# Kernel optimization log

Measured on AMD Instinct MI355X. Metric: run time of the kernel, lower is better.

Reference implementation:

```python
import jax, jax.numpy as jnp
import numpy as np

B, IMG, P, CIN, D, L, H, HID = 64, 224, 16, 3, 768, 12, 12, 3072
HD = D // H                      # 64 head dim
N = (IMG // P) ** 2 + 1          # 197 tokens (cls + patches)
EQ = 1.0 / np.sqrt(D)            # EqualLinear scale (lr_mul=1)


def _ln(x):
    # LayerNorm(eps=1e-3, elementwise_affine=False)
    m = jnp.mean(x, axis=-1, keepdims=True)
    v = jnp.var(x, axis=-1, keepdims=True)
    return (x - m) * jax.lax.rsqrt(v + 1e-3)


def _smln(x, latent, gw, gb, bw, bb):
    # SelfModulatedLayerNorm: param-free LN then per-sample affine from latent
    gamma = (latent @ (gw * EQ).T + gb)[:, None, :]
    beta = (latent @ (bw * EQ).T + bb)[:, None, :]
    return _ln(x) * (1.0 + gamma) + beta


def _attention(x, qkvw, projw, projb):
    b, n, d = x.shape
    qkv = (x @ qkvw.T).reshape(b, n, 3, H, HD).transpose(2, 0, 3, 1, 4)  # [3,B,H,N,hd]
    q, k, v = qkv[0], qkv[1], qkv[2]
    attn = jax.nn.softmax(jnp.einsum('bhqd,bhkd->bhqk', q, k) * (HD ** -0.5), axis=-1)
    out = jnp.einsum('bhqk,bhkd->bhqd', attn, v).transpose(0, 2, 1, 3).reshape(b, n, d)
    return out @ projw.T + projb


def _forward(x, latent, conv_w, conv_b, cls_token, pos_embed,
             g1w, g1b, b1w, b1b, qkvw, projw, projb,
             g2w, g2b, b2w, b2b, fc1w, fc1b, fc2w, fc2b,
             gnw, gnb, bnw, bnb):
    b = x.shape[0]
    # PatchEmbed: conv stride=patch, flatten, transpose, sin activation
    feat = jax.lax.conv_general_dilated(
        x, conv_w, (P, P), 'VALID',
        dimension_numbers=('NCHW', 'OIHW', 'NCHW')) + conv_b[None, :, None, None]
    tok = jnp.sin(feat.reshape(b, D, -1).transpose(0, 2, 1))          # [B,196,D]
    tok = jnp.concatenate([jnp.broadcast_to(cls_token, (b, 1, D)), tok], axis=1)
    tok = tok + pos_embed                                             # [B,197,D]

    def block(t, p):
        (g1w_, g1b_, b1w_, b1b_, qkvw_, projw_, projb_,
         g2w_, g2b_, b2w_, b2b_, fc1w_, fc1b_, fc2w_, fc2b_) = p
        xn = _smln(t, latent, g1w_, g1b_, b1w_, b1b_)
        y = _attention(xn, qkvw_, projw_, projb_) + xn
        t = xn + y                       # source Block: x reassigned to norm1 output
        t = _smln(t, latent, g2w_, g2b_, b2w_, b2b_)
        h = jax.nn.gelu(t @ fc1w_.T + fc1b_, approximate=False)
        t = (h @ fc2w_.T + fc2b_) + t
        return t, None

    tok, _ = jax.lax.scan(block, tok, (g1w, g1b, b1w, b1b, qkvw, projw, projb,
                                       g2w, g2b, b2w, b2b, fc1w, fc1b, fc2w, fc2b))
    return _smln(tok, latent, gnw, gnb, bnw, bnb)


def setup_inputs() -> dict:
    key = jax.random.key(0)
    ks = jax.random.split(key, 20)
    r = lambda k, shape: 0.02 * jax.random.normal(k, shape, dtype=jnp.float32)
    z = lambda shape: jnp.zeros(shape, jnp.float32)
    return {
        'x': jax.random.normal(ks[0], (B, CIN, IMG, IMG), dtype=jnp.float32),
        'latent': jax.random.normal(ks[1], (B, D), dtype=jnp.float32),
        'conv_w': r(ks[2], (D, CIN, P, P)), 'conv_b': z((D,)),
        'cls_token': z((1, 1, D)), 'pos_embed': r(ks[3], (1, N, D)),
        'g1w': r(ks[4], (L, D, D)), 'g1b': z((L, D)),
        'b1w': r(ks[5], (L, D, D)), 'b1b': z((L, D)),
        'qkvw': r(ks[6], (L, 3 * D, D)),
        'projw': r(ks[7], (L, D, D)), 'projb': z((L, D)),
        'g2w': r(ks[8], (L, D, D)), 'g2b': z((L, D)),
        'b2w': r(ks[9], (L, D, D)), 'b2b': z((L, D)),
        'fc1w': r(ks[10], (L, HID, D)), 'fc1b': z((L, HID)),
        'fc2w': r(ks[11], (L, D, HID)), 'fc2b': z((L, D)),
        'gnw': r(ks[12], (D, D)), 'gnb': z((D,)),
        'bnw': r(ks[13], (D, D)), 'bnb': z((D,)),
    }


def reference(x, latent, conv_w, conv_b, cls_token, pos_embed,
              g1w, g1b, b1w, b1b, qkvw, projw, projb,
              g2w, g2b, b2w, b2b, fc1w, fc1b, fc2w, fc2b,
              gnw, gnb, bnw, bnb):
    return _forward(x, latent, conv_w, conv_b, cls_token, pos_embed,
                    g1w, g1b, b1w, b1b, qkvw, projw, projb,
                    g2w, g2b, b2w, b2b, fc1w, fc1b, fc2w, fc2b,
                    gnw, gnb, bnw, bnb)
```

## Files before the change

### kernel.cpp

```cpp
#include <hip/hip_runtime.h>

typedef unsigned short u16;
typedef __bf16 bf16x8 __attribute__((ext_vector_type(8)));
typedef unsigned short u16x8 __attribute__((ext_vector_type(8)));
typedef float f32x4 __attribute__((ext_vector_type(4)));

#define B_    64
#define NTOK  197
#define DIM   768
#define NH    12
#define LAY   12
#define HID_  3072
#define MROWS (B_*NTOK)

#define EPI_BF16  0
#define EPI_PROJ  2
#define EPI_GELU  3
#define EPI_FC2   4
#define EPI_PATCH 5

__device__ __forceinline__ u16 f2bf(float f) {
  unsigned u = __float_as_uint(f);
  u += 0x7FFFu + ((u >> 16) & 1u);
  return (u16)(u >> 16);
}
__device__ __forceinline__ float bf2f(u16 h) {
  return __uint_as_float(((unsigned)h) << 16);
}

__device__ __forceinline__ void gld_lds16(const void* g, void* l) {
  __builtin_amdgcn_global_load_lds(
      (const __attribute__((address_space(1))) void*)g,
      (__attribute__((address_space(3))) void*)l, 16, 0, 0);
}

__global__ void fill_k(float* __restrict__ o, float v, int n) {
  int i = blockIdx.x * blockDim.x + threadIdx.x;
  const int st = gridDim.x * blockDim.x;
  for (; i < n; i += st) o[i] = v;
}

__global__ void cvt_bf16(const float* __restrict__ in, u16* __restrict__ out, int n4) {
  int i = blockIdx.x * blockDim.x + threadIdx.x;
  const int st = gridDim.x * blockDim.x;
  for (; i < n4; i += st) {
    float4 v = ((const float4*)in)[i];
    ushort4 o;
    o.x = f2bf(v.x); o.y = f2bf(v.y); o.z = f2bf(v.z); o.w = f2bf(v.w);
    ((ushort4*)out)[i] = o;
  }
}

__global__ void cvt4_k(const float* __restrict__ s0, const float* __restrict__ s1,
                       const float* __restrict__ s2, const float* __restrict__ s3,
                       u16* __restrict__ d0, u16* __restrict__ d1,
                       u16* __restrict__ d2, u16* __restrict__ d3,
                       int n0, int n1, int n2, int n3)
{
  int i = blockIdx.x * blockDim.x + threadIdx.x;
  const int st = gridDim.x * blockDim.x;
  const int total = n0 + n1 + n2 + n3;
  for (; i < total; i += st) {
    const float* s; u16* d; int j = i;
    if (j < n0) { s = s0; d = d0; }
    else { j -= n0;
      if (j < n1) { s = s1; d = d1; }
      else { j -= n1;
        if (j < n2) { s = s2; d = d2; }
        else { j -= n2; s = s3; d = d3; } } }
    float4 v = ((const float4*)s)[j];
    ushort4 o;
    o.x = f2bf(v.x); o.y = f2bf(v.y); o.z = f2bf(v.z); o.w = f2bf(v.w);
    ((ushort4*)d)[j] = o;
  }
}

__global__ void im2col_k(const float* __restrict__ x, u16* __restrict__ out) {
  int i = blockIdx.x * blockDim.x + threadIdx.x;
  const int st = gridDim.x * blockDim.x;
  const int total = 12544 * 768;
  for (; i < total; i += st) {
    int row = i / 768, col = i - row * 768;
    int b = row / 196, pr = row - b * 196;
    int py = pr / 14, px = pr - py * 14;
    int cin = col >> 8, rr = col & 255;
    int ky = rr >> 4, kx = rr & 15;
    out[i] = f2bf(x[((b * 3 + cin) * 224 + py * 16 + ky) * 224 + px * 16 + kx]);
  }
}

__global__ void clspos_k(const float* __restrict__ cls, const float* __restrict__ pos,
                         float* __restrict__ t) {
  int i = blockIdx.x * blockDim.x + threadIdx.x;
  if (i >= B_ * DIM) return;
  int b = i / DIM, d = i - b * DIM;
  t[(size_t)b * NTOK * DIM + d] = cls[d] + pos[d];
}

__global__ __launch_bounds__(256)
void modk(const float* __restrict__ lat, const float* __restrict__ w,
          const float* __restrict__ bias, float* __restrict__ out, int ldb)
{
  __shared__ float ls[32][65];
  __shared__ float wsm[64][33];
  const int tid = threadIdx.x;
  const int mat = blockIdx.y;
  const int n0 = blockIdx.x * 64;
  const int nl = tid & 63;
  const int bg = tid >> 6;
  float acc[16];
  #pragma unroll
  for (int j = 0; j < 16; ++j) acc[j] = 0.f;
  for (int k0 = 0; k0 < 768; k0 += 32) {
    __syncthreads();
    #pragma unroll
    for (int i = 0; i < 8; ++i) {
      int idx = tid + i * 256;
      int rr = idx >> 5, kk = idx & 31;
      ls[kk][rr]  = lat[rr * 768 + k0 + kk];
      wsm[rr][kk] = w[((size_t)mat * 768 + n0 + rr) * 768 + k0 + kk];
    }
    __syncthreads();
    #pragma unroll 4
    for (int kk = 0; kk < 32; ++kk) {
      float wv = wsm[nl][kk];
      #pragma unroll
      for (int j = 0; j < 16; ++j)
        acc[j] += ls[kk][bg * 16 + j] * wv;
    }
  }
  const float EQS = 0.036084391824351615f;
  const float* bs = bias + (size_t)mat * 768 + n0;
  #pragma unroll
  for (int j = 0; j < 16; ++j) {
    int b = bg * 16 + j;
    out[(size_t)b * ldb + mat * 768 + n0 + nl] = acc[j] * EQS + bs[nl];
  }
}

__global__ __launch_bounds__(256)
void smln_k(const float* __restrict__ x,
            const float* __restrict__ gamma, const float* __restrict__ beta, int ldg,
            float* __restrict__ oF, u16* __restrict__ oB)
{
  const int row = blockIdx.x;
  const int tid = threadIdx.x;
  const float* xr = x + (size_t)row * DIM;
  float v0 = xr[tid], v1 = xr[tid + 256], v2 = xr[tid + 512];
  float s1 = v0 + v1 + v2;
  float s2 = v0 * v0 + v1 * v1 + v2 * v2;
  #pragma unroll
  for (int o = 32; o; o >>= 1) { s1 += __shfl_xor(s1, o); s2 += __shfl_xor(s2, o); }
  __shared__ float rs[8];
  const int lane = tid & 63, wv = tid >> 6;
  if (lane == 0) { rs[wv] = s1; rs[4 + wv] = s2; }
  __syncthreads();
  s1 = rs[0] + rs[1] + rs[2] + rs[3];
  s2 = rs[4] + rs[5] + rs[6] + rs[7];
  const float mean = s1 * (1.f / 768.f);
  const float var  = s2 * (1.f / 768.f) - mean * mean;
  const float rstd = rsqrtf(var + 1e-3f);
  const int b = row / NTOK;
  const float* g  = gamma + (size_t)b * ldg;
  const float* be = beta  + (size_t)b * ldg;
  const size_t base = (size_t)row * DIM;
  float vv[3] = {v0, v1, v2};
  #pragma unroll
  for (int j = 0; j < 3; ++j) {
    int d = tid + j * 256;
    float y = (vv[j] - mean) * rstd;
    y = y * (1.f + g[d]) + be[d];
    if (oF) oF[base + d] = y;
    if (oB) oB[base + d] = f2bf(y);
  }
}

__global__ __launch_bounds__(256)
void attn_k(const u16* __restrict__ qkv, u16* __restrict__ ao)
{
  __shared__ u16 Ks[208 * 68];
  __shared__ u16 Vt[64 * 226];
  __shared__ u16 Ps[4][16 * 228];
  const int bh = blockIdx.x;
  const int b = bh / NH, h = bh - (bh / NH) * NH;
  const int tid = threadIdx.x;
  const int lane = tid & 63, wv = tid >> 6;
  const int lr = lane & 15, kg = lane >> 4;
  const size_t tb = (size_t)(b * NTOK) * 2304 + h * 64;

  for (int t = tid; t < 1576; t += 256) {
    int n = t >> 3, c = t & 7;
    *(u16x8*)&Ks[n * 68 + c * 8] =
        *(const u16x8*)&qkv[tb + (size_t)n * 2304 + 768 + c * 8];
  }
  for (int t = tid; t < 1576; t += 256) {
    int n = t >> 3, dc = t & 7;
    u16x8 v = *(const u16x8*)&qkv[tb + (size_t)n * 2304 + 1536 + dc * 8];
    #pragma unroll
    for (int j = 0; j < 8; ++j) Vt[(dc * 8 + j) * 226 + n] = v[j];
  }
  for (int i = tid; i < 11 * 68; i += 256) Ks[197 * 68 + i] = 0;
  for (int i = tid; i < 64 * 29; i += 256) {
    int d = i / 29, c = i - d * 29;
    Vt[d * 226 + 197 + c] = 0;
  }
  for (int i = tid; i < 4 * 16 * 20; i += 256) {
    int w = i / 320, rm = i - w * 320, r = rm / 20, c = rm - r * 20;
    Ps[w][r * 228 + 208 + c] = 0;
  }
  __syncthreads();

  const f32x4 z4 = {0.f, 0.f, 0.f, 0.f};
  u16* pw = Ps[wv];

  for (int qt = wv; qt < 13; qt += 4) {
    const int q0 = qt * 16;
    const int qrow = min(q0 + lr, 196);
    const bf16x8 aq0 = *(const bf16x8*)&qkv[tb + (size_t)qrow * 2304 + kg * 8];
    const bf16x8 aq1 = *(const bf16x8*)&qkv[tb + (size_t)qrow * 2304 + 32 + kg * 8];

    f32x4 acc[13];
    #pragma unroll
    for (int ct = 0; ct < 13; ++ct) acc[ct] = z4;
    #pragma unroll
    for (int ct = 0; ct < 13; ++ct) {
      const bf16x8 bk0 = *(const bf16x8*)&Ks[(ct * 16 + lr) * 68 + kg * 8];
      const bf16x8 bk1 = *(const bf16x8*)&Ks[(ct * 16 + lr) * 68 + 32 + kg * 8];
      acc[ct] = __builtin_amdgcn_mfma_f32_16x16x32_bf16(aq0, bk0, acc[ct], 0, 0, 0);
      acc[ct] = __builtin_amdgcn_mfma_f32_16x16x32_bf16(aq1, bk1, acc[ct], 0, 0, 0);
    }

    float mx[4], sm[4], inv[4];
    #pragma unroll
    for (int r = 0; r < 4; ++r) mx[r] = -1e30f;
    #pragma unroll
    for (int ct = 0; ct < 13; ++ct)
      #pragma unroll
      for (int r = 0; r < 4; ++r) {
        float s = acc[ct][r] * 0.125f;
        if (ct * 16 + lr >= 197) s = -1e30f;
        acc[ct][r] = s;
        mx[r] = fmaxf(mx[r], s);
      }
    #pragma unroll
    for (int o = 1; o < 16; o <<= 1)
      #pragma unroll
      for (int r = 0; r < 4; ++r) mx[r] = fmaxf(mx[r], __shfl_xor(mx[r], o));
    #pragma unroll
    for (int r = 0; r < 4; ++r) sm[r] = 0.f;
    #pragma unroll
    for (int ct = 0; ct < 13; ++ct)
      #pragma unroll
      for (int r = 0; r < 4; ++r) {
        float p = __expf(acc[ct][r] - mx[r]);
        acc[ct][r] = p;
        sm[r] += p;
      }
    #pragma unroll
    for (int o = 1; o < 16; o <<= 1)
      #pragma unroll
      for (int r = 0; r < 4; ++r) sm[r] += __shfl_xor(sm[r], o);
    #pragma unroll
    for (int r = 0; r < 4; ++r) inv[r] = 1.f / sm[r];

    #pragma unroll
    for (int ct = 0; ct < 13; ++ct)
      #pragma unroll
      for (int r = 0; r < 4; ++r)
        pw[(kg * 4 + r) * 228 + ct * 16 + lr] = f2bf(acc[ct][r]);
    asm volatile("s_waitcnt lgkmcnt(0)" ::: "memory");
    __builtin_amdgcn_sched_barrier(0);

    f32x4 accO[4];
    #pragma unroll
    for (int dt = 0; dt < 4; ++dt) accO[dt] = z4;
    #pragma unroll
    for (int kt = 0; kt < 7; ++kt) {
      const bf16x8 ap = *(const bf16x8*)&pw[lr * 228 + kt * 32 + kg * 8];
      #pragma unroll
      for (int dt = 0; dt < 4; ++dt) {
        const bf16x8 bv = *(const bf16x8*)&Vt[(dt * 16 + lr) * 226 + kt * 32 + kg * 8];
        accO[dt] = __builtin_amdgcn_mfma_f32_16x16x32_bf16(ap, bv, accO[dt], 0, 0, 0);
      }
    }

    #pragma unroll
    for (int r = 0; r < 4; ++r) {
      const int q = q0 + kg * 4 + r;
      if (q < NTOK) {
        const size_t base = ((size_t)(b * NTOK + q)) * DIM + h * 64;
        #pragma unroll
        for (int dt = 0; dt < 4; ++dt)
          ao[base + dt * 16 + lr] = f2bf(accO[dt][r] * inv[r]);
      }
    }
  }
}

template<int EPI>
__global__ __launch_bounds__(256)
void gemm_bt(const u16* __restrict__ A, int lda,
             const u16* __restrict__ Bw, int ldb,
             int M, int K, int gn,
             const float* __restrict__ bias,
             const u16* __restrict__ res,
             float* __restrict__ outF, u16* __restrict__ outB, int ldo,
             const float* __restrict__ aux)
{
  __shared__ u16 SA[3][4096];
  __shared__ u16 SB[3][4096];
  const int tid = threadIdx.x;
  const int lane = tid & 63, wv = tid >> 6;
  const int lr = lane & 15, kg = lane >> 4;
  const int wm = wv >> 1, wn = wv & 1;

  const int nwg = gridDim.x;
  const int qq = nwg >> 3, rr2 = nwg & 7;
  const int xcd = blockIdx.x & 7, loc = blockIdx.x >> 3;
  const int v = (xcd < rr2 ? xcd * (qq + 1) : rr2 * (qq + 1) + (xcd - rr2) * qq) + loc;
  const int tm = v / gn, tn = v - tm * gn;

  const int c0 = tid, c1 = tid + 256;
  const int r0 = c0 >> 2, q0 = (c0 & 3) ^ (r0 & 3) ^ ((r0 >> 2) & 3);
  const int r1 = c1 >> 2, q1 = (c1 & 3) ^ (r1 & 3) ^ ((r1 >> 2) & 3);
  int am0 = tm * 128 + r0; if (am0 >= M) am0 = M - 1;
  int am1 = tm * 128 + r1; if (am1 >= M) am1 = M - 1;
  const u16* aS0 = A  + (size_t)am0 * lda + q0 * 8;
  const u16* aS1 = A  + (size_t)am1 * lda + q1 * 8;
  const u16* bS0 = Bw + (size_t)(tn * 128 + r0) * ldb + q0 * 8;
  const u16* bS1 = Bw + (size_t)(tn * 128 + r1) * ldb + q1 * 8;

  f32x4 acc[4][4];
  const f32x4 z = {0.f, 0.f, 0.f, 0.f};
  #pragma unroll
  for (int m = 0; m < 4; ++m)
    #pragma unroll
    for (int n = 0; n < 4; ++n) acc[m][n] = z;

#define STG(buf, ko) do { \
    u16* aD = &SA[buf][wv * 512]; u16* bD = &SB[buf][wv * 512]; \
    gld_lds16(aS0 + (ko), aD);        gld_lds16(aS1 + (ko), aD + 2048); \
    gld_lds16(bS0 + (ko), bD);        gld_lds16(bS1 + (ko), bD + 2048); \
  } while (0)

  const int KT = K >> 5;
  STG(0, 0);
  STG(1, 32);
  asm volatile("s_waitcnt vmcnt(4)" ::: "memory");
  __builtin_amdgcn_s_barrier();

  #pragma unroll 1
  for (int t0 = 0; t0 < KT; t0 += 3) {
    #pragma unroll
    for (int u = 0; u < 3; ++u) {
      const int t = t0 + u;
      if (t) {
        asm volatile("s_waitcnt lgkmcnt(0)" ::: "memory");
        if (t + 1 < KT) asm volatile("s_waitcnt vmcnt(4)" ::: "memory");
        else            asm volatile("s_waitcnt vmcnt(0)" ::: "memory");
        __builtin_amdgcn_s_barrier();
      }
      if (t + 2 < KT) STG((u + 2) % 3, (t + 2) * 32);
      bf16x8 af[4], bfr[4];
      #pragma unroll
      for (int m = 0; m < 4; ++m) {
        int row = wm * 64 + m * 16 + lr;
        af[m] = *(const bf16x8*)&SA[u][row * 32 + (((kg ^ row ^ (row >> 2)) & 3) << 3)];
      }
      #pragma unroll
      for (int n = 0; n < 4; ++n) {
        int row = wn * 64 + n * 16 + lr;
        bfr[n] = *(const bf16x8*)&SB[u][row * 32 + (((kg ^ row ^ (row >> 2)) & 3) << 3)];
      }
      #pragma unroll
      for (int m = 0; m < 4; ++m)
        #pragma unroll
        for (int n = 0; n < 4; ++n)
          acc[m][n] = __builtin_amdgcn_mfma_f32_16x16x32_bf16(af[m], bfr[n], acc[m][n], 0, 0, 0);
    }
  }
#undef STG
  __syncthreads();

  const int gr0 = tm * 128 + wm * 64;
  const int gc0 = tn * 128 + wn * 64;
  if constexpr (EPI == EPI_BF16 || EPI == EPI_GELU) {
    u16* T = (u16*)SA + wv * 1152;
    #pragma unroll
    for (int m = 0; m < 4; ++m) {
      #pragma unroll
      for (int n = 0; n < 4; ++n) {
        #pragma unroll
        for (int r = 0; r < 4; ++r) {
          float val = acc[m][n][r];
          if constexpr (EPI == EPI_GELU) {
            float u = val + bias[gc0 + n * 16 + lr];
            val = 0.5f * u * (1.f + erff(u * 0.70710678118654752f));
          }
          T[(kg * 4 + r) * 72 + n * 16 + lr] = f2bf(val);
        }
      }
      asm volatile("s_waitcnt lgkmcnt(0)" ::: "memory");
      __builtin_amdgcn_sched_barrier(0);
      #pragma unroll
      for (int half = 0; half < 2; ++half) {
        int row = (lane >> 3) + half * 8;
        int c8 = lane & 7;
        u16x8 vv = *(const u16x8*)&T[row * 72 + c8 * 8];
        int gr = gr0 + m * 16 + row;
        if (gr < M) *(u16x8*)&outB[(size_t)gr * ldo + gc0 + c8 * 8] = vv;
      }
      asm volatile("s_waitcnt lgkmcnt(0)" ::: "memory");
      __builtin_amdgcn_sched_barrier(0);
    }
  } else {
    float* T = (float*)SA + wv * 1088;
    #pragma unroll
    for (int m = 0; m < 4; ++m) {
      #pragma unroll
      for (int n = 0; n < 4; ++n)
        #pragma unroll
        for (int r = 0; r < 4; ++r)
          T[(kg * 4 + r) * 68 + n * 16 + lr] = acc[m][n][r];
      asm volatile("s_waitcnt lgkmcnt(0)" ::: "memory");
      __builtin_amdgcn_sched_barrier(0);
      #pragma unroll
      for (int qu = 0; qu < 4; ++qu) {
        int row = (lane >> 4) + qu * 4;
        int c4 = lane & 15;
        f32x4 vv = *(const f32x4*)&T[row * 68 + c4 * 4];
        int gr = gr0 + m * 16 + row;
        int gc = gc0 + c4 * 4;
        if (gr < M) {
          f32x4 bv = *(const f32x4*)&bias[gc];
          if constexpr (EPI == EPI_PROJ) {
            size_t o = (size_t)gr * ldo + gc;
            ushort4 rv = *(const ushort4*)&res[o];
            f32x4 ov;
            ov[0] = vv[0] + bv[0] + 2.f * bf2f(rv.x);
            ov[1] = vv[1] + bv[1] + 2.f * bf2f(rv.y);
            ov[2] = vv[2] + bv[2] + 2.f * bf2f(rv.z);
            ov[3] = vv[3] + bv[3] + 2.f * bf2f(rv.w);
            *(f32x4*)&outF[o] = ov;
          } else if constexpr (EPI == EPI_FC2) {
            size_t o = (size_t)gr * ldo + gc;
            ushort4 rv = *(const ushort4*)&res[o];
            f32x4 ov;
            ov[0] = vv[0] + bv[0] + bf2f(rv.x);
            ov[1] = vv[1] + bv[1] + bf2f(rv.y);
            ov[2] = vv[2] + bv[2] + bf2f(rv.z);
            ov[3] = vv[3] + bv[3] + bf2f(rv.w);
            *(f32x4*)&outF[o] = ov;
          } else {
            int pb = gr / 196, pp = gr - pb * 196;
            size_t o = ((size_t)pb * NTOK + 1 + pp) * DIM + gc;
            f32x4 av = *(const f32x4*)&aux[(size_t)(1 + pp) * DIM + gc];
            f32x4 ov;
            #pragma unroll
            for (int j = 0; j < 4; ++j) ov[j] = sinf(vv[j] + bv[j]) + av[j];
            *(f32x4*)&outF[o] = ov;
          }
        }
      }
      asm volatile("s_waitcnt lgkmcnt(0)" ::: "memory");
      __builtin_amdgcn_sched_barrier(0);
    }
  }
}

extern "C" void kernel_launch(void* const* d_in, const int* in_sizes, int n_in,
                              void* d_out, int out_size, void* d_ws, size_t ws_size,
                              hipStream_t stream)
{
  (void)in_sizes; (void)n_in;
  const float* X     = (const float*)d_in[0];
  const float* LAT   = (const float*)d_in[1];
  const float* CONVW = (const float*)d_in[2];
  const float* CONVB = (const float*)d_in[3];
  const float* CLS   = (const float*)d_in[4];
  const float* POS   = (const float*)d_in[5];
  const float* G1W   = (const float*)d_in[6];
  const float* G1B   = (const float*)d_in[7];
  const float* B1W   = (const float*)d_in[8];
  const float* B1B   = (const float*)d_in[9];
  const float* QKVW  = (const float*)d_in[10];
  const float* PROJW = (const float*)d_in[11];
  const float* PROJB = (const float*)d_in[12];
  const float* G2W   = (const float*)d_in[13];
  const float* G2B   = (const float*)d_in[14];
  const float* B2W   = (const float*)d_in[15];
  const float* B2B   = (const float*)d_in[16];
  const float* FC1W  = (const float*)d_in[17];
  const float* FC1B  = (const float*)d_in[18];
  const float* FC2W  = (const float*)d_in[19];
  const float* FC2B  = (const float*)d_in[20];
  const float* GNW   = (const float*)d_in[21];
  const float* GNB   = (const float*)d_in[22];
  const float* BNW   = (const float*)d_in[23];
  const float* BNB   = (const float*)d_in[24];

  char* p = (char*)d_ws;
  auto carve = [&](size_t bytes) { char* r = p; p += (bytes + 255) & ~(size_t)255; return r; };

  char* Ubuf  = carve((size_t)MROWS * HID_ * 2);
  u16* patches = (u16*)Ubuf;
  u16* qkvb    = (u16*)Ubuf;
  u16* hb      = (u16*)Ubuf;
  u16* wconv  = (u16*)carve((size_t)768 * 768 * 2);
  u16* wqkv_l = (u16*)carve((size_t)2304 * 768 * 2);
  u16* wproj_l= (u16*)carve((size_t)768 * 768 * 2);
  u16* wfc1_l = (u16*)carve((size_t)3072 * 768 * 2);
  u16* wfc2_l = (u16*)carve((size_t)768 * 3072 * 2);
  float* tf   = (float*)carve((size_t)MROWS * 768 * 4);
  u16* xnb    = (u16*)carve((size_t)MROWS * 768 * 2);
  u16* aob    = (u16*)carve((size_t)MROWS * 768 * 2);
  float* gam1 = (float*)carve((size_t)B_ * 9216 * 4);
  float* bet1 = (float*)carve((size_t)B_ * 9216 * 4);
  float* gam2 = (float*)carve((size_t)B_ * 9216 * 4);
  float* bet2 = (float*)carve((size_t)B_ * 9216 * 4);
  float* gamN = (float*)carve((size_t)B_ * 768 * 4);
  float* betN = (float*)carve((size_t)B_ * 768 * 4);

  fill_k<<<1, 64, 0, stream>>>((float*)d_out, 1e9f, 1);
  if ((size_t)(p - (char*)d_ws) > ws_size) {
    fill_k<<<256, 256, 0, stream>>>((float*)d_out, 1e9f, out_size);
    return;
  }

  modk<<<dim3(12, 12), 256, 0, stream>>>(LAT, G1W, G1B, gam1, 9216);
  modk<<<dim3(12, 12), 256, 0, stream>>>(LAT, B1W, B1B, bet1, 9216);
  modk<<<dim3(12, 12), 256, 0, stream>>>(LAT, G2W, G2B, gam2, 9216);
  modk<<<dim3(12, 12), 256, 0, stream>>>(LAT, B2W, B2B, bet2, 9216);
  modk<<<dim3(12, 1),  256, 0, stream>>>(LAT, GNW, GNB, gamN, 768);
  modk<<<dim3(12, 1),  256, 0, stream>>>(LAT, BNW, BNB, betN, 768);

  {
    int n4 = 768 * 768 / 4;
    cvt_bf16<<<(n4 + 255) / 256, 256, 0, stream>>>(CONVW, wconv, n4);
  }
  im2col_k<<<4096, 256, 0, stream>>>(X, patches);
  gemm_bt<EPI_PATCH><<<98 * 6, 256, 0, stream>>>(patches, 768, wconv, 768, 12544, 768, 6,
                                                 CONVB, nullptr, tf, nullptr, 768, POS);
  clspos_k<<<(B_ * DIM + 255) / 256, 256, 0, stream>>>(CLS, POS, tf);

  const int n4_qkv = 2304 * 768 / 4, n4_pro = 768 * 768 / 4, n4_fc = 3072 * 768 / 4;
  for (int l = 0; l < LAY; ++l) {
    cvt4_k<<<4096, 256, 0, stream>>>(QKVW + (size_t)l * 2304 * 768, PROJW + (size_t)l * 768 * 768,
                                     FC1W + (size_t)l * 3072 * 768, FC2W + (size_t)l * 768 * 3072,
                                     wqkv_l, wproj_l, wfc1_l, wfc2_l,
                                     n4_qkv, n4_pro, n4_fc, n4_fc);
    smln_k<<<MROWS, 256, 0, stream>>>(tf, gam1 + l * 768, bet1 + l * 768, 9216, nullptr, xnb);
    gemm_bt<EPI_BF16><<<99 * 18, 256, 0, stream>>>(xnb, 768, wqkv_l, 768, MROWS, 768, 18,
                                                   nullptr, nullptr, nullptr, qkvb, 2304, nullptr);
    attn_k<<<B_ * NH, 256, 0, stream>>>(qkvb, aob);
    gemm_bt<EPI_PROJ><<<99 * 6, 256, 0, stream>>>(aob, 768, wproj_l, 768, MROWS, 768, 6,
                                                  PROJB + l * 768, xnb, tf, nullptr, 768, nullptr);
    smln_k<<<MROWS, 256, 0, stream>>>(tf, gam2 + l * 768, bet2 + l * 768, 9216, nullptr, xnb);
    gemm_bt<EPI_GELU><<<99 * 24, 256, 0, stream>>>(xnb, 768, wfc1_l, 768, MROWS, 768, 24,
                                                   FC1B + l * 3072, nullptr, nullptr, hb, 3072, nullptr);
    gemm_bt<EPI_FC2><<<99 * 6, 256, 0, stream>>>(hb, 3072, wfc2_l, 3072, MROWS, 3072, 6,
                                                 FC2B + l * 768, xnb, tf, nullptr, 768, nullptr);
  }
  smln_k<<<MROWS, 256, 0, stream>>>(tf, gamN, betN, 768, (float*)d_out, nullptr);
}
```

Baseline: 6.746 ms.

## Switch GEMMs to 256x256 tiles with 512 threads and phased double-buffered pipeline

Replaces the 128x128, 256-thread GEMM with a 256x256-tile, 512-thread kernel that uses a K-step of 64 and double-buffered LDS. Each K-tile is split into four phases that interleave global-to-LDS prefetch of the next tile with MFMA work, raising wave priority during the matrix math. The goal is more operand reuse per byte loaded and better overlap of loads with compute. The trade-off is that the larger tiles give far fewer workgroups: 150 for the proj and fc2 GEMMs, fewer than the CU count, which risks leaving CUs idle. The 128 KB of LDS per block also limits occupancy.

```diff
diff --git a/kernel.cpp b/kernel.cpp
--- a/kernel.cpp
+++ b/kernel.cpp
@@ -298,8 +298,8 @@
 }
 
 template<int EPI>
-__global__ __launch_bounds__(256)
-void gemm_bt(const u16* __restrict__ A, int lda,
+__global__ __launch_bounds__(512, 2)
+void gemm256(const u16* __restrict__ A, int lda,
              const u16* __restrict__ Bw, int ldb,
              int M, int K, int gn,
              const float* __restrict__ bias,
@@ -307,12 +307,12 @@
              float* __restrict__ outF, u16* __restrict__ outB, int ldo,
              const float* __restrict__ aux)
 {
-  __shared__ u16 SA[3][4096];
-  __shared__ u16 SB[3][4096];
+  __shared__ u16 SA[2][16384];
+  __shared__ u16 SB[2][16384];
   const int tid = threadIdx.x;
   const int lane = tid & 63, wv = tid >> 6;
   const int lr = lane & 15, kg = lane >> 4;
-  const int wm = wv >> 1, wn = wv & 1;
+  const int wm = wv >> 2, wn = wv & 3;
 
   const int nwg = gridDim.x;
   const int qq = nwg >> 3, rr2 = nwg & 7;
@@ -320,74 +320,116 @@
   const int v = (xcd < rr2 ? xcd * (qq + 1) : rr2 * (qq + 1) + (xcd - rr2) * qq) + loc;
   const int tm = v / gn, tn = v - tm * gn;
 
-  const int c0 = tid, c1 = tid + 256;
-  const int r0 = c0 >> 2, q0 = (c0 & 3) ^ (r0 & 3) ^ ((r0 >> 2) & 3);
-  const int r1 = c1 >> 2, q1 = (c1 & 3) ^ (r1 & 3) ^ ((r1 >> 2) & 3);
-  int am0 = tm * 128 + r0; if (am0 >= M) am0 = M - 1;
-  int am1 = tm * 128 + r1; if (am1 >= M) am1 = M - 1;
-  const u16* aS0 = A  + (size_t)am0 * lda + q0 * 8;
-  const u16* aS1 = A  + (size_t)am1 * lda + q1 * 8;
-  const u16* bS0 = Bw + (size_t)(tn * 128 + r0) * ldb + q0 * 8;
-  const u16* bS1 = Bw + (size_t)(tn * 128 + r1) * ldb + q1 * 8;
-
-  f32x4 acc[4][4];
+  const u16* aSrc[4];
+  const u16* bSrc[4];
+  #pragma unroll
+  for (int j = 0; j < 4; ++j) {
+    int c = tid + j * 512;
+    int r = c >> 3, q = (c & 7) ^ (r & 7);
+    int am = tm * 256 + r; if (am >= M) am = M - 1;
+    aSrc[j] = A  + (size_t)am * lda + q * 8;
+    bSrc[j] = Bw + (size_t)(tn * 256 + r) * ldb + q * 8;
+  }
+
+#define SGA(BUF, J, KO) gld_lds16(aSrc[J] + (KO), &SA[BUF][((J) * 512 + wv * 64) * 8])
+#define SGB(BUF, J, KO) gld_lds16(bSrc[J] + (KO), &SB[BUF][((J) * 512 + wv * 64) * 8])
+
+  f32x4 acc[8][4];
   const f32x4 z = {0.f, 0.f, 0.f, 0.f};
   #pragma unroll
-  for (int m = 0; m < 4; ++m)
+  for (int m = 0; m < 8; ++m)
     #pragma unroll
     for (int n = 0; n < 4; ++n) acc[m][n] = z;
 
-#define STG(buf, ko) do { \
-    u16* aD = &SA[buf][wv * 512]; u16* bD = &SB[buf][wv * 512]; \
-    gld_lds16(aS0 + (ko), aD);        gld_lds16(aS1 + (ko), aD + 2048); \
-    gld_lds16(bS0 + (ko), bD);        gld_lds16(bS1 + (ko), bD + 2048); \
+  const int KT = K >> 6;
+
+  SGB(0, 0, 0); SGB(0, 1, 0); SGB(0, 2, 0); SGB(0, 3, 0);
+  SGA(0, 0, 0); SGA(0, 2, 0); SGA(0, 1, 0); SGA(0, 3, 0);
+  asm volatile("s_waitcnt vmcnt(2)" ::: "memory");
+  __builtin_amdgcn_s_barrier();
+
+#define RDA(BUF, P) \
+    _Pragma("unroll") \
+    for (int ks = 0; ks < 2; ++ks) \
+      _Pragma("unroll") \
+      for (int mm = 0; mm < 2; ++mm) { \
+        int rrow = wm * 128 + ((P) * 2 + mm) * 16 + lr; \
+        af[ks][mm] = *(const bf16x8*)&SA[BUF][rrow * 64 + ((((ks * 4 + kg) ^ (rrow & 7))) << 3)]; \
+      }
+
+#define MM(P) \
+    _Pragma("unroll") \
+    for (int ks = 0; ks < 2; ++ks) \
+      _Pragma("unroll") \
+      for (int mm = 0; mm < 2; ++mm) \
+        _Pragma("unroll") \
+        for (int n = 0; n < 4; ++n) \
+          acc[(P) * 2 + mm][n] = __builtin_amdgcn_mfma_f32_16x16x32_bf16( \
+              af[ks][mm], bfr[ks][n], acc[(P) * 2 + mm][n], 0, 0, 0);
+
+#define TILE(BUF) do { \
+    const int ko = (kt + 1) * 64; \
+    const bool pf = (kt + 1 < KT); \
+    bf16x8 bfr[2][4]; \
+    bf16x8 af[2][2]; \
+     \
+    _Pragma("unroll") \
+    for (int ks = 0; ks < 2; ++ks) \
+      _Pragma("unroll") \
+      for (int n = 0; n < 4; ++n) { \
+        int rrow = wn * 64 + n * 16 + lr; \
+        bfr[ks][n] = *(const bf16x8*)&SB[BUF][rrow * 64 + ((((ks * 4 + kg) ^ (rrow & 7))) << 3)]; \
+      } \
+    RDA(BUF, 0); \
+    if (pf) { SGB(BUF ^ 1, 0, ko); SGB(BUF ^ 1, 1, ko); } \
+    __builtin_amdgcn_s_barrier(); \
+    asm volatile("s_waitcnt lgkmcnt(0)" ::: "memory"); \
+    __builtin_amdgcn_s_setprio(1); MM(0); __builtin_amdgcn_s_setprio(0); \
+    __builtin_amdgcn_s_barrier(); \
+     \
+    RDA(BUF, 1); \
+    if (pf) { SGB(BUF ^ 1, 2, ko); SGB(BUF ^ 1, 3, ko); } \
+    __builtin_amdgcn_s_barrier(); \
+    asm volatile("s_waitcnt lgkmcnt(0)" ::: "memory"); \
+    __builtin_amdgcn_s_setprio(1); MM(1); __builtin_amdgcn_s_setprio(0); \
+    if (pf) { asm volatile("s_waitcnt vmcnt(4)" ::: "memory"); } \
+    else    { asm volatile("s_waitcnt vmcnt(0)" ::: "memory"); } \
+    __builtin_amdgcn_s_barrier(); \
+     \
+    RDA(BUF, 2); \
+    if (pf) { SGA(BUF ^ 1, 0, ko); SGA(BUF ^ 1, 2, ko); } \
+    __builtin_amdgcn_s_barrier(); \
+    asm volatile("s_waitcnt lgkmcnt(0)" ::: "memory"); \
+    __builtin_amdgcn_s_setprio(1); MM(2); __builtin_amdgcn_s_setprio(0); \
+    __builtin_amdgcn_s_barrier(); \
+     \
+    RDA(BUF, 3); \
+    if (pf) { SGA(BUF ^ 1, 1, ko); SGA(BUF ^ 1, 3, ko); } \
+    __builtin_amdgcn_s_barrier(); \
+    asm volatile("s_waitcnt lgkmcnt(0)" ::: "memory"); \
+    __builtin_amdgcn_s_setprio(1); MM(3); __builtin_amdgcn_s_setprio(0); \
+    if (pf) { asm volatile("s_waitcnt vmcnt(2)" ::: "memory"); } \
+    else    { asm volatile("s_waitcnt vmcnt(0)" ::: "memory"); } \
+    __builtin_amdgcn_s_barrier(); \
   } while (0)
 
-  const int KT = K >> 5;
-  STG(0, 0);
-  STG(1, 32);
-  asm volatile("s_waitcnt vmcnt(4)" ::: "memory");
-  __builtin_amdgcn_s_barrier();
-
-  #pragma unroll 1
-  for (int t0 = 0; t0 < KT; t0 += 3) {
-    #pragma unroll
-    for (int u = 0; u < 3; ++u) {
-      const int t = t0 + u;
-      if (t) {
-        asm volatile("s_waitcnt lgkmcnt(0)" ::: "memory");
-        if (t + 1 < KT) asm volatile("s_waitcnt vmcnt(4)" ::: "memory");
-        else            asm volatile("s_waitcnt vmcnt(0)" ::: "memory");
-        __builtin_amdgcn_s_barrier();
-      }
-      if (t + 2 < KT) STG((u + 2) % 3, (t + 2) * 32);
-      bf16x8 af[4], bfr[4];
-      #pragma unroll
-      for (int m = 0; m < 4; ++m) {
-        int row = wm * 64 + m * 16 + lr;
-        af[m] = *(const bf16x8*)&SA[u][row * 32 + (((kg ^ row ^ (row >> 2)) & 3) << 3)];
-      }
-      #pragma unroll
-      for (int n = 0; n < 4; ++n) {
-        int row = wn * 64 + n * 16 + lr;
-        bfr[n] = *(const bf16x8*)&SB[u][row * 32 + (((kg ^ row ^ (row >> 2)) & 3) << 3)];
-      }
-      #pragma unroll
-      for (int m = 0; m < 4; ++m)
-        #pragma unroll
-        for (int n = 0; n < 4; ++n)
-          acc[m][n] = __builtin_amdgcn_mfma_f32_16x16x32_bf16(af[m], bfr[n], acc[m][n], 0, 0, 0);
-    }
-  }
-#undef STG
+  for (int kt0 = 0; kt0 < KT; kt0 += 2) {
+    { const int kt = kt0;     TILE(0); }
+    { const int kt = kt0 + 1; TILE(1); }
+  }
+#undef TILE
+#undef MM
+#undef RDA
+#undef SGA
+#undef SGB
   __syncthreads();
 
-  const int gr0 = tm * 128 + wm * 64;
-  const int gc0 = tn * 128 + wn * 64;
+  const int gr0 = tm * 256 + wm * 128;
+  const int gc0 = tn * 256 + wn * 64;
   if constexpr (EPI == EPI_BF16 || EPI == EPI_GELU) {
     u16* T = (u16*)SA + wv * 1152;
     #pragma unroll
-    for (int m = 0; m < 4; ++m) {
+    for (int m = 0; m < 8; ++m) {
       #pragma unroll
       for (int n = 0; n < 4; ++n) {
         #pragma unroll
@@ -416,7 +458,7 @@
   } else {
     float* T = (float*)SA + wv * 1088;
     #pragma unroll
-    for (int m = 0; m < 4; ++m) {
+    for (int m = 0; m < 8; ++m) {
       #pragma unroll
       for (int n = 0; n < 4; ++n)
         #pragma unroll
@@ -539,8 +581,8 @@
     cvt_bf16<<<(n4 + 255) / 256, 256, 0, stream>>>(CONVW, wconv, n4);
   }
   im2col_k<<<4096, 256, 0, stream>>>(X, patches);
-  gemm_bt<EPI_PATCH><<<98 * 6, 256, 0, stream>>>(patches, 768, wconv, 768, 12544, 768, 6,
-                                                 CONVB, nullptr, tf, nullptr, 768, POS);
+  gemm256<EPI_PATCH><<<147, 512, 0, stream>>>(patches, 768, wconv, 768, 12544, 768, 3,
+                                              CONVB, nullptr, tf, nullptr, 768, POS);
   clspos_k<<<(B_ * DIM + 255) / 256, 256, 0, stream>>>(CLS, POS, tf);
 
   const int n4_qkv = 2304 * 768 / 4, n4_pro = 768 * 768 / 4, n4_fc = 3072 * 768 / 4;
@@ -550,16 +592,16 @@
                                      wqkv_l, wproj_l, wfc1_l, wfc2_l,
                                      n4_qkv, n4_pro, n4_fc, n4_fc);
     smln_k<<<MROWS, 256, 0, stream>>>(tf, gam1 + l * 768, bet1 + l * 768, 9216, nullptr, xnb);
-    gemm_bt<EPI_BF16><<<99 * 18, 256, 0, stream>>>(xnb, 768, wqkv_l, 768, MROWS, 768, 18,
-                                                   nullptr, nullptr, nullptr, qkvb, 2304, nullptr);
+    gemm256<EPI_BF16><<<450, 512, 0, stream>>>(xnb, 768, wqkv_l, 768, MROWS, 768, 9,
+                                               nullptr, nullptr, nullptr, qkvb, 2304, nullptr);
     attn_k<<<B_ * NH, 256, 0, stream>>>(qkvb, aob);
-    gemm_bt<EPI_PROJ><<<99 * 6, 256, 0, stream>>>(aob, 768, wproj_l, 768, MROWS, 768, 6,
-                                                  PROJB + l * 768, xnb, tf, nullptr, 768, nullptr);
+    gemm256<EPI_PROJ><<<150, 512, 0, stream>>>(aob, 768, wproj_l, 768, MROWS, 768, 3,
+                                               PROJB + l * 768, xnb, tf, nullptr, 768, nullptr);
     smln_k<<<MROWS, 256, 0, stream>>>(tf, gam2 + l * 768, bet2 + l * 768, 9216, nullptr, xnb);
-    gemm_bt<EPI_GELU><<<99 * 24, 256, 0, stream>>>(xnb, 768, wfc1_l, 768, MROWS, 768, 24,
-                                                   FC1B + l * 3072, nullptr, nullptr, hb, 3072, nullptr);
-    gemm_bt<EPI_FC2><<<99 * 6, 256, 0, stream>>>(hb, 3072, wfc2_l, 3072, MROWS, 3072, 6,
-                                                 FC2B + l * 768, xnb, tf, nullptr, 768, nullptr);
+    gemm256<EPI_GELU><<<600, 512, 0, stream>>>(xnb, 768, wfc1_l, 768, MROWS, 768, 12,
+                                               FC1B + l * 3072, nullptr, nullptr, hb, 3072, nullptr);
+    gemm256<EPI_FC2><<<150, 512, 0, stream>>>(hb, 3072, wfc2_l, 3072, MROWS, 3072, 3,
+                                              FC2B + l * 768, xnb, tf, nullptr, 768, nullptr);
   }
   smln_k<<<MROWS, 256, 0, stream>>>(tf, gamN, betN, 768, (float*)d_out, nullptr);
 }
```

After: 6.622 ms. About the same (-1.8%).
